# Kernel tuning notes

Measured on AMD Instinct MI355X. Metric: run time of the kernel, lower is better.

The kernel has to match this reference:

```python
import jax, jax.numpy as jnp
import numpy as np

N_NODES = 100000
N_EDGES = 1600000
N_GRAPH = 100
IN_DIM = 64
LATENT = 128
STEPS = 2
MLP_LAYERS = 2
OUT_GLOBALS = 1
EPS = 1e-5  # haiku LayerNorm default


def setup_inputs() -> dict:
    key = jax.random.key(0)
    ks = jax.random.split(key, 8)
    nodes = jax.random.normal(ks[0], (N_NODES, IN_DIM), jnp.float32)
    senders = jax.random.randint(ks[1], (N_EDGES,), 0, N_NODES, jnp.int32)
    receivers = jax.random.randint(ks[2], (N_EDGES,), 0, N_NODES, jnp.int32)
    # 100 graphs of 1000 nodes each: jnp.repeat(arange(n_graph), n_node)
    graph_ids = (jnp.arange(N_NODES) // (N_NODES // N_GRAPH)).astype(jnp.int32)
    embed_w = jax.random.normal(ks[3], (IN_DIM, LATENT), jnp.float32) / np.sqrt(IN_DIM).astype(np.float32)
    embed_b = jnp.zeros((LATENT,), jnp.float32)
    mlp_w = jax.random.normal(ks[4], (STEPS, MLP_LAYERS, LATENT, LATENT), jnp.float32) / np.sqrt(LATENT).astype(np.float32)
    mlp_b = jnp.zeros((STEPS, MLP_LAYERS, LATENT), jnp.float32)
    ln_scale = jnp.ones((STEPS, LATENT), jnp.float32)
    ln_offset = jnp.zeros((STEPS, LATENT), jnp.float32)
    dec_w = jax.random.normal(ks[5], (LATENT, OUT_GLOBALS), jnp.float32) / np.sqrt(LATENT).astype(np.float32)
    dec_b = jnp.zeros((OUT_GLOBALS,), jnp.float32)
    return dict(nodes=nodes, senders=senders, receivers=receivers, graph_ids=graph_ids,
                embed_w=embed_w, embed_b=embed_b, mlp_w=mlp_w, mlp_b=mlp_b,
                ln_scale=ln_scale, ln_offset=ln_offset, dec_w=dec_w, dec_b=dec_b)


def _layernorm(x, scale, offset):
    mu = jnp.mean(x, axis=-1, keepdims=True)
    var = jnp.var(x, axis=-1, keepdims=True)
    return (x - mu) * jax.lax.rsqrt(var + EPS) * scale + offset


def reference(nodes, senders, receivers, graph_ids, embed_w, embed_b,
              mlp_w, mlp_b, ln_scale, ln_offset, dec_w, dec_b):
    n = nodes.shape[0]
    # jraph.GraphConvolution(add_self_edges=True, symmetric_normalization=True)
    self_loop = jnp.arange(n, dtype=senders.dtype)
    conv_s = jnp.concatenate([senders, self_loop])
    conv_r = jnp.concatenate([receivers, self_loop])
    ones_e = jnp.ones(conv_s.shape[0], jnp.float32)
    inv_sqrt_sdeg = jax.lax.rsqrt(jnp.maximum(jax.ops.segment_sum(ones_e, conv_s, n), 1.0))
    inv_sqrt_rdeg = jax.lax.rsqrt(jnp.maximum(jax.ops.segment_sum(ones_e, conv_r, n), 1.0))

    # embedder: hk.Linear on nodes
    h = nodes @ embed_w + embed_b

    for s in range(STEPS):
        # update_node_fn: MLP (dropout_rate=0 -> identity dropout)
        x = h
        for l in range(MLP_LAYERS):
            x = jax.nn.relu(x @ mlp_w[s, l] + mlp_b[s, l])
        # symmetric-normalized segment_sum aggregation with self-edges
        x = x * inv_sqrt_sdeg[:, None]
        x = jax.ops.segment_sum(x[conv_s], conv_r, num_segments=n)  # [n, LATENT]
        x = x * inv_sqrt_rdeg[:, None]
        h = x + h  # skip connection (add_graphs_tuples)
        h = _layernorm(h, ln_scale[s], ln_offset[s])

    # segment_mean pooling over graphs
    counts = jnp.maximum(jax.ops.segment_sum(jnp.ones(n, jnp.float32), graph_ids, N_GRAPH), 1.0)
    pooled = jax.ops.segment_sum(h, graph_ids, num_segments=N_GRAPH) / counts[:, None]
    # decoder: hk.Linear on pooled globals
    return pooled @ dec_w + dec_b  # [N_GRAPH, OUT_GLOBALS]
```

## Files before the change

### kernel.cpp

```cpp
#include <hip/hip_runtime.h>
#include <hip/hip_bf16.h>


#define N_NODES 100000
#define N_EDGES 1600000
#define N_GRAPH 100
#define NPG     1000
#define LATENT  128

#define NPART   8
#define PSIZE   (N_NODES / NPART)
#define NSLICE  32
#define ESLICE  (N_EDGES / NSLICE)

#define SCAN_CHUNK 2048
#define SCAN_NB    ((N_NODES + SCAN_CHUNK - 1) / SCAN_CHUNK)

#define PCHUNK  20
#define PCNODES (NPG / PCHUNK)

typedef __attribute__((ext_vector_type(8))) short short8;
typedef __attribute__((ext_vector_type(4))) float f32x4;

__device__ __forceinline__ unsigned short f2bf(float f) {
    union { float f; unsigned int u; } v; v.f = f;
    unsigned int r = v.u + 0x7fff + ((v.u >> 16) & 1);
    return (unsigned short)(r >> 16);
}
__device__ __forceinline__ float bf2f(unsigned short u) {
    union { unsigned int u; float f; } v; v.u = ((unsigned int)u) << 16;
    return v.f;
}

__global__ __launch_bounds__(1024) void k_hist2(const int* __restrict__ senders,
                                                const int* __restrict__ receivers,
                                                int* __restrict__ ps,
                                                int* __restrict__ pr) {
    __shared__ int cs[PSIZE];
    __shared__ int cr[PSIZE];
    int rg = blockIdx.x & (NPART - 1), sl = blockIdx.x >> 3;
    int lo = rg * PSIZE;
    for (int i = threadIdx.x; i < PSIZE; i += 1024) { cs[i] = 0; cr[i] = 0; }
    __syncthreads();
    int e0 = sl * ESLICE;
    for (int e = e0 + threadIdx.x; e < e0 + ESLICE; e += 1024) {
        int s = senders[e] - lo;
        if ((unsigned)s < PSIZE) atomicAdd(&cs[s], 1);
        int r = receivers[e] - lo;
        if ((unsigned)r < PSIZE) atomicAdd(&cr[r], 1);
    }
    __syncthreads();
    int base = (rg * NSLICE + sl) * PSIZE;
    for (int i = threadIdx.x; i < PSIZE; i += 1024) {
        ps[base + i] = cs[i];
        pr[base + i] = cr[i];
    }
}

__global__ __launch_bounds__(256) void k_scan_slices(const int* __restrict__ ps,
                                                     int* __restrict__ pr,
                                                     int* __restrict__ deg_r,
                                                     float* __restrict__ inv_s,
                                                     float* __restrict__ inv_r) {
    int n = blockIdx.x * 256 + threadIdx.x;
    if (n >= N_NODES) return;
    int rg = n / PSIZE, i = n - rg * PSIZE;
    size_t base = (size_t)rg * NSLICE * PSIZE + i;
    int run = 0, ss = 0;
#pragma unroll 4
    for (int sl = 0; sl < NSLICE; sl++) {
        size_t idx = base + (size_t)sl * PSIZE;
        int v = pr[idx];
        pr[idx] = run;
        run += v;
        ss += ps[idx];
    }
    deg_r[n] = run;
    inv_r[n] = rsqrtf((float)(run + 1));
    inv_s[n] = rsqrtf((float)(ss + 1));
}

__global__ __launch_bounds__(256) void k_scan_block(const int* __restrict__ deg,
                                                    int* __restrict__ blocksums, int n) {
    int b = blockIdx.x, t = threadIdx.x;
    int base = b * SCAN_CHUNK + t * 8;
    int s = 0;
#pragma unroll
    for (int j = 0; j < 8; j++) { int i = base + j; if (i < n) s += deg[i]; }
    __shared__ int wsum[4];
#pragma unroll
    for (int off = 32; off > 0; off >>= 1) s += __shfl_down(s, off, 64);
    if ((t & 63) == 0) wsum[t >> 6] = s;
    __syncthreads();
    if (t == 0) blocksums[b] = wsum[0] + wsum[1] + wsum[2] + wsum[3];
}

__global__ __launch_bounds__(64) void k_scan_top(int* __restrict__ blocksums, int nb) {
    int t = threadIdx.x;
    int v = (t < nb) ? blocksums[t] : 0;
    int inc = v;
#pragma unroll
    for (int off = 1; off < 64; off <<= 1) {
        int u = __shfl_up(inc, off, 64);
        if (t >= off) inc += u;
    }
    if (t < nb) blocksums[t] = inc - v;
}

__global__ __launch_bounds__(256) void k_scan_apply(const int* __restrict__ deg,
                                                    const int* __restrict__ blockoffs,
                                                    int* __restrict__ row_start, int n) {
    int b = blockIdx.x, t = threadIdx.x;
    int base = b * SCAN_CHUNK + t * 8;
    int v[8]; int tsum = 0;
#pragma unroll
    for (int j = 0; j < 8; j++) { int i = base + j; v[j] = (i < n) ? deg[i] : 0; tsum += v[j]; }
    __shared__ int wtot[4];
    int inc = tsum;
#pragma unroll
    for (int off = 1; off < 64; off <<= 1) {
        int u = __shfl_up(inc, off, 64);
        if ((t & 63) >= off) inc += u;
    }
    if ((t & 63) == 63) wtot[t >> 6] = inc;
    __syncthreads();
    int wbase = 0;
    for (int w = 0; w < (t >> 6); w++) wbase += wtot[w];
    int running = blockoffs[b] + wbase + (inc - tsum);
#pragma unroll
    for (int j = 0; j < 8; j++) {
        int i = base + j;
        if (i < n) {
            row_start[i] = running;
            running += v[j];
            if (i == n - 1) row_start[n] = running;
        }
    }
}

__global__ void k_mkbase(int* __restrict__ pr, const int* __restrict__ row_start) {
    int idx = blockIdx.x * 256 + threadIdx.x;
    if (idx >= NPART * NSLICE * PSIZE) return;
    int rg = idx / (NSLICE * PSIZE);
    int i = idx % PSIZE;
    pr[idx] += row_start[rg * PSIZE + i];
}

__global__ __launch_bounds__(1024) void k_fill2(const int* __restrict__ senders,
                                                const int* __restrict__ receivers,
                                                const int* __restrict__ baseoff,
                                                int* __restrict__ edge_src) {
    __shared__ int bs[PSIZE];
    int rg = blockIdx.x & (NPART - 1), sl = blockIdx.x >> 3;
    int lo = rg * PSIZE;
    const int* base = baseoff + (size_t)(rg * NSLICE + sl) * PSIZE;
    for (int i = threadIdx.x; i < PSIZE; i += 1024) bs[i] = base[i];
    __syncthreads();
    int e0 = sl * ESLICE;
    for (int e = e0 + threadIdx.x; e < e0 + ESLICE; e += 1024) {
        int r = receivers[e] - lo;
        if ((unsigned)r < PSIZE) {
            int pos = atomicAdd(&bs[r], 1);
            edge_src[pos] = senders[e];
        }
    }
}

__global__ void k_wprep(const float* __restrict__ embed_w, const float* __restrict__ mlp_w,
                        unsigned short* __restrict__ hi, unsigned short* __restrict__ lo) {
    int t = blockIdx.x * 256 + threadIdx.x;
    if (t >= 8192 + 4 * 16384) return;
    const float* src; int local;
    if (t < 8192) { src = embed_w; local = t; }
    else { int m = t - 8192; src = mlp_w + (size_t)(m >> 14) * 16384; local = m & 16383; }
    int j = local & 7, lane = (local >> 3) & 63, tn = (local >> 9) & 7, kc = local >> 12;
    int k = kc * 32 + ((lane >> 4) << 3) + j;
    int n = tn * 16 + (lane & 15);
    float wv = src[k * 128 + n];
    unsigned short h = f2bf(wv);
    float rem = wv - bf2f(h);
    hi[t] = h; lo[t] = f2bf(rem);
}

__global__ __launch_bounds__(256) void k_embed(
    const float* __restrict__ A, const unsigned short* __restrict__ wfhi,
    const unsigned short* __restrict__ wflo, const float* __restrict__ eb,
    unsigned short* __restrict__ h16, int M)
{
    __shared__ __align__(16) unsigned short t0[4][32][136];
    int t = threadIdx.x, w = t >> 6, L = t & 63;
    int m0 = blockIdx.x * 128 + w * 32;
    int lr = L & 15, lk = (L >> 4) * 8, lq = (L >> 4) * 4;

    float ebv[8];
#pragma unroll
    for (int tn = 0; tn < 8; tn++) ebv[tn] = eb[tn * 16 + lr];

    f32x4 acc[2][8];
#pragma unroll
    for (int bd = 0; bd < 2; bd++)
#pragma unroll
        for (int tn = 0; tn < 8; tn++) acc[bd][tn] = (f32x4){0.f, 0.f, 0.f, 0.f};

#pragma unroll
    for (int kc = 0; kc < 2; kc++) {
        short8 a[2];
#pragma unroll
        for (int bd = 0; bd < 2; bd++) {
            int grow = m0 + bd * 16 + lr; if (grow >= M) grow = M - 1;
            const float* rp = A + (size_t)grow * 64 + kc * 32 + lk;
            float4 v0 = *(const float4*)rp;
            float4 v1 = *(const float4*)(rp + 4);
            short8 pk;
            pk[0] = (short)f2bf(v0.x); pk[1] = (short)f2bf(v0.y);
            pk[2] = (short)f2bf(v0.z); pk[3] = (short)f2bf(v0.w);
            pk[4] = (short)f2bf(v1.x); pk[5] = (short)f2bf(v1.y);
            pk[6] = (short)f2bf(v1.z); pk[7] = (short)f2bf(v1.w);
            a[bd] = pk;
        }
#pragma unroll
        for (int tn = 0; tn < 8; tn++) {
            size_t fo = (size_t)(((kc * 8 + tn) * 64 + L)) * 8;
            short8 bh = *(const short8*)(wfhi + fo);
            short8 bl = *(const short8*)(wflo + fo);
#pragma unroll
            for (int bd = 0; bd < 2; bd++) {
                acc[bd][tn] = __builtin_amdgcn_mfma_f32_16x16x32_bf16(a[bd], bh, acc[bd][tn], 0, 0, 0);
                acc[bd][tn] = __builtin_amdgcn_mfma_f32_16x16x32_bf16(a[bd], bl, acc[bd][tn], 0, 0, 0);
            }
        }
    }
#pragma unroll
    for (int bd = 0; bd < 2; bd++)
#pragma unroll
        for (int tn = 0; tn < 8; tn++)
#pragma unroll
            for (int r = 0; r < 4; r++)
                t0[w][bd * 16 + lq + r][tn * 16 + lr] = f2bf(acc[bd][tn][r] + ebv[tn]);
#pragma unroll
    for (int q = 0; q < 8; q++) {
        int s = q * 64 + L;
        int row = s >> 4, c0 = (s & 15) * 8;
        int grow = m0 + row;
        if (grow < M)
            *(short8*)(h16 + (size_t)grow * 128 + c0) = *(const short8*)&t0[w][row][c0];
    }
}

__global__ __launch_bounds__(256) void k_mlp(
    const unsigned short* __restrict__ A16, const unsigned short* __restrict__ w0hi,
    const unsigned short* __restrict__ w0lo, const unsigned short* __restrict__ w1hi,
    const unsigned short* __restrict__ w1lo, const float* __restrict__ b0,
    const float* __restrict__ b1, const float* __restrict__ inv_s,
    unsigned short* __restrict__ x16, int M)
{
    __shared__ __align__(16) unsigned short t1[4][32][136];
    int t = threadIdx.x, w = t >> 6, L = t & 63;
    int m0 = blockIdx.x * 128 + w * 32;
    int lr = L & 15, lk = (L >> 4) * 8, lq = (L >> 4) * 4;

    float b0v[8], b1v[8];
#pragma unroll
    for (int tn = 0; tn < 8; tn++) { b0v[tn] = b0[tn * 16 + lr]; b1v[tn] = b1[tn * 16 + lr]; }

    f32x4 acc[2][8];
#pragma unroll
    for (int bd = 0; bd < 2; bd++)
#pragma unroll
        for (int tn = 0; tn < 8; tn++) acc[bd][tn] = (f32x4){0.f, 0.f, 0.f, 0.f};

#pragma unroll
    for (int kc = 0; kc < 4; kc++) {
        short8 a[2];
#pragma unroll
        for (int bd = 0; bd < 2; bd++) {
            int grow = m0 + bd * 16 + lr; if (grow >= M) grow = M - 1;
            a[bd] = *(const short8*)(A16 + (size_t)grow * 128 + kc * 32 + lk);
        }
#pragma unroll
        for (int tn = 0; tn < 8; tn++) {
            size_t fo = (size_t)(((kc * 8 + tn) * 64 + L)) * 8;
            short8 bh = *(const short8*)(w0hi + fo);
            short8 bl = *(const short8*)(w0lo + fo);
#pragma unroll
            for (int bd = 0; bd < 2; bd++) {
                acc[bd][tn] = __builtin_amdgcn_mfma_f32_16x16x32_bf16(a[bd], bh, acc[bd][tn], 0, 0, 0);
                acc[bd][tn] = __builtin_amdgcn_mfma_f32_16x16x32_bf16(a[bd], bl, acc[bd][tn], 0, 0, 0);
            }
        }
    }
#pragma unroll
    for (int bd = 0; bd < 2; bd++)
#pragma unroll
        for (int tn = 0; tn < 8; tn++)
#pragma unroll
            for (int r = 0; r < 4; r++) {
                float v = acc[bd][tn][r] + b0v[tn];
                v = fmaxf(v, 0.f);
                t1[w][bd * 16 + lq + r][tn * 16 + lr] = f2bf(v);
            }

    f32x4 acc2[2][8];
#pragma unroll
    for (int bd = 0; bd < 2; bd++)
#pragma unroll
        for (int tn = 0; tn < 8; tn++) acc2[bd][tn] = (f32x4){0.f, 0.f, 0.f, 0.f};

#pragma unroll
    for (int kc = 0; kc < 4; kc++) {
        short8 a[2];
#pragma unroll
        for (int bd = 0; bd < 2; bd++)
            a[bd] = *(const short8*)&t1[w][bd * 16 + lr][kc * 32 + lk];
#pragma unroll
        for (int tn = 0; tn < 8; tn++) {
            size_t fo = (size_t)(((kc * 8 + tn) * 64 + L)) * 8;
            short8 bh = *(const short8*)(w1hi + fo);
            short8 bl = *(const short8*)(w1lo + fo);
#pragma unroll
            for (int bd = 0; bd < 2; bd++) {
                acc2[bd][tn] = __builtin_amdgcn_mfma_f32_16x16x32_bf16(a[bd], bh, acc2[bd][tn], 0, 0, 0);
                acc2[bd][tn] = __builtin_amdgcn_mfma_f32_16x16x32_bf16(a[bd], bl, acc2[bd][tn], 0, 0, 0);
            }
        }
    }

    float invs[2][4];
#pragma unroll
    for (int bd = 0; bd < 2; bd++)
#pragma unroll
        for (int r = 0; r < 4; r++) {
            int grow = m0 + bd * 16 + lq + r; if (grow >= M) grow = M - 1;
            invs[bd][r] = inv_s[grow];
        }
#pragma unroll
    for (int bd = 0; bd < 2; bd++)
#pragma unroll
        for (int tn = 0; tn < 8; tn++)
#pragma unroll
            for (int r = 0; r < 4; r++) {
                float v = acc2[bd][tn][r] + b1v[tn];
                v = fmaxf(v, 0.f) * invs[bd][r];
                t1[w][bd * 16 + lq + r][tn * 16 + lr] = f2bf(v);
            }
#pragma unroll
    for (int q = 0; q < 8; q++) {
        int s = q * 64 + L;
        int row = s >> 4;
        int c0 = (s & 15) * 8;
        int grow = m0 + row;
        if (grow < M)
            *(short8*)(x16 + (size_t)grow * 128 + c0) = *(const short8*)&t1[w][row][c0];
    }
}

__global__ __launch_bounds__(256) void k_agg_ln(
    const unsigned short* __restrict__ x16, const int* __restrict__ row_start,
    const int* __restrict__ edge_src, const float* __restrict__ inv_r,
    const float* __restrict__ ln_scale, const float* __restrict__ ln_offset,
    unsigned short* __restrict__ h16)
{
    int node = __builtin_amdgcn_readfirstlane(blockIdx.x * 4 + (threadIdx.x >> 6));
    int L = threadIdx.x & 63;
    const unsigned int* x32 = (const unsigned int*)x16;
    const unsigned int* h32 = (const unsigned int*)h16;

    unsigned int su = x32[(size_t)node * 64 + L];
    float a0 = bf2f((unsigned short)(su & 0xffff));
    float a1 = bf2f((unsigned short)(su >> 16));

    int beg = row_start[node], end = row_start[node + 1];
    int j = beg;
    for (; j + 8 <= end; j += 8) {
        unsigned int u[8];
#pragma unroll
        for (int q = 0; q < 8; q++) u[q] = x32[(size_t)edge_src[j + q] * 64 + L];
#pragma unroll
        for (int q = 0; q < 8; q++) {
            a0 += bf2f((unsigned short)(u[q] & 0xffff));
            a1 += bf2f((unsigned short)(u[q] >> 16));
        }
    }
    for (; j < end; j++) {
        unsigned int u0 = x32[(size_t)edge_src[j] * 64 + L];
        a0 += bf2f((unsigned short)(u0 & 0xffff));
        a1 += bf2f((unsigned short)(u0 >> 16));
    }

    float ir = inv_r[node];
    unsigned int hu = h32[(size_t)node * 64 + L];
    float y0 = a0 * ir + bf2f((unsigned short)(hu & 0xffff));
    float y1 = a1 * ir + bf2f((unsigned short)(hu >> 16));

    float s1 = y0 + y1, s2 = y0 * y0 + y1 * y1;
#pragma unroll
    for (int off = 32; off > 0; off >>= 1) {
        s1 += __shfl_xor(s1, off, 64);
        s2 += __shfl_xor(s2, off, 64);
    }
    float mu = s1 * (1.f / 128.f);
    float var = fmaxf(s2 * (1.f / 128.f) - mu * mu, 0.f);
    float rstd = rsqrtf(var + 1e-5f);
    float2 sc = *(const float2*)&ln_scale[L * 2];
    float2 of = *(const float2*)&ln_offset[L * 2];
    float ox = (y0 - mu) * rstd * sc.x + of.x;
    float oy = (y1 - mu) * rstd * sc.y + of.y;
    ((unsigned int*)h16)[(size_t)node * 64 + L] =
        (unsigned int)f2bf(ox) | ((unsigned int)f2bf(oy) << 16);
}

__global__ __launch_bounds__(256) void k_pool1(const unsigned short* __restrict__ h16,
                                               float* __restrict__ partial) {
    int b = blockIdx.x;
    int g = b / PCHUNK, c = b % PCHUNK;
    int t = threadIdx.x, col = t & 127, half = t >> 7;
    const unsigned short* hg = h16 + ((size_t)g * NPG + (size_t)c * PCNODES) * 128;
    float acc = 0.f;
    for (int i = half; i < PCNODES; i += 2) acc += bf2f(hg[(size_t)i * 128 + col]);
    __shared__ float red[256];
    red[t] = acc;
    __syncthreads();
    if (half == 0) partial[(size_t)b * 128 + col] = red[col] + red[col + 128];
}

__global__ __launch_bounds__(128) void k_pool2(const float* __restrict__ partial,
                                               const float* __restrict__ dec_w,
                                               const float* __restrict__ dec_b,
                                               float* __restrict__ out) {
    int g = blockIdx.x, col = threadIdx.x;
    const float* pg = partial + (size_t)g * PCHUNK * 128;
    float s = 0.f;
#pragma unroll
    for (int c = 0; c < PCHUNK; c++) s += pg[c * 128 + col];
    s = s * (1.f / (float)NPG) * dec_w[col];
    __shared__ float ws[2];
#pragma unroll
    for (int off = 32; off > 0; off >>= 1) s += __shfl_down(s, off, 64);
    if ((col & 63) == 0) ws[col >> 6] = s;
    __syncthreads();
    if (col == 0) out[g] = ws[0] + ws[1] + dec_b[0];
}

extern "C" void kernel_launch(void* const* d_in, const int* in_sizes, int n_in,
                              void* d_out, int out_size, void* d_ws, size_t ws_size,
                              hipStream_t stream) {
    (void)in_sizes; (void)n_in; (void)out_size; (void)ws_size;
    const float* nodes     = (const float*)d_in[0];
    const int*   senders   = (const int*)d_in[1];
    const int*   receivers = (const int*)d_in[2];
    const float* embed_w   = (const float*)d_in[4];
    const float* embed_b   = (const float*)d_in[5];
    const float* mlp_w     = (const float*)d_in[6];
    const float* mlp_b     = (const float*)d_in[7];
    const float* ln_scale  = (const float*)d_in[8];
    const float* ln_offset = (const float*)d_in[9];
    const float* dec_w     = (const float*)d_in[10];
    const float* dec_b     = (const float*)d_in[11];
    float* out = (float*)d_out;

    const int N = N_NODES;
    const int WF_TOTAL = 8192 + 4 * 16384;
    const int PART_TOTAL = NPART * NSLICE * PSIZE;

    char* p = (char*)d_ws;
    auto alloc = [&](size_t bytes) -> void* {
        void* r = (void*)p;
        p += (bytes + 255) & ~(size_t)255;
        return r;
    };
    unsigned short* h16      = (unsigned short*)alloc((size_t)N * 128 * 2);
    unsigned short* x16      = (unsigned short*)alloc((size_t)N * 128 * 2);
    int*            edge_src = (int*)alloc((size_t)N_EDGES * 4);
    int*            ps       = (int*)alloc((size_t)PART_TOTAL * 4);
    int*            pr       = (int*)alloc((size_t)PART_TOTAL * 4);
    int*            deg_r    = (int*)alloc((size_t)N * 4);
    float*          inv_s    = (float*)alloc((size_t)N * 4);
    float*          inv_r    = (float*)alloc((size_t)N * 4);
    int*            row_start= (int*)alloc((size_t)(N + 1) * 4);
    int*            blocksums= (int*)alloc((size_t)SCAN_NB * 4);
    unsigned short* wfhi     = (unsigned short*)alloc((size_t)WF_TOTAL * 2);
    unsigned short* wflo     = (unsigned short*)alloc((size_t)WF_TOTAL * 2);
    float*          poolpart = (float*)alloc((size_t)N_GRAPH * PCHUNK * 128 * 4);

    k_wprep<<<(WF_TOTAL + 255) / 256, 256, 0, stream>>>(embed_w, mlp_w, wfhi, wflo);

    k_hist2<<<NPART * NSLICE, 1024, 0, stream>>>(senders, receivers, ps, pr);
    k_scan_slices<<<(N + 255) / 256, 256, 0, stream>>>(ps, pr, deg_r, inv_s, inv_r);
    k_scan_block<<<SCAN_NB, 256, 0, stream>>>(deg_r, blocksums, N);
    k_scan_top<<<1, 64, 0, stream>>>(blocksums, SCAN_NB);
    k_scan_apply<<<SCAN_NB, 256, 0, stream>>>(deg_r, blocksums, row_start, N);
    k_mkbase<<<(PART_TOTAL + 255) / 256, 256, 0, stream>>>(pr, row_start);
    k_fill2<<<NPART * NSLICE, 1024, 0, stream>>>(senders, receivers, pr, edge_src);

    int mblocks = (N + 127) / 128;
    k_embed<<<mblocks, 256, 0, stream>>>(nodes, wfhi, wflo, embed_b, h16, N);

    for (int s = 0; s < 2; s++) {
        const unsigned short* w0hi = wfhi + 8192 + (size_t)(s * 2 + 0) * 16384;
        const unsigned short* w0lo = wflo + 8192 + (size_t)(s * 2 + 0) * 16384;
        const unsigned short* w1hi = wfhi + 8192 + (size_t)(s * 2 + 1) * 16384;
        const unsigned short* w1lo = wflo + 8192 + (size_t)(s * 2 + 1) * 16384;
        const float* b0 = mlp_b + (size_t)(s * 2 + 0) * 128;
        const float* b1 = mlp_b + (size_t)(s * 2 + 1) * 128;
        k_mlp<<<mblocks, 256, 0, stream>>>(h16, w0hi, w0lo, w1hi, w1lo, b0, b1, inv_s, x16, N);
        k_agg_ln<<<N / 4, 256, 0, stream>>>(x16, row_start, edge_src, inv_r,
                                            ln_scale + (size_t)s * 128,
                                            ln_offset + (size_t)s * 128, h16);
    }

    k_pool1<<<N_GRAPH * PCHUNK, 256, 0, stream>>>(h16, poolpart);
    k_pool2<<<N_GRAPH, 128, 0, stream>>>(poolpart, dec_w, dec_b, out);
}
```

Baseline: 436.4 us.

## Fuse embedder into first MLP step, shrink partition counters to u16, drop mkbase

The embedding GEMM and the step-0 two-layer MLP now run in one kernel. The embedded tile stays in LDS as the A operand, so the separate reload of h16 is avoided. Per-slice histogram counters are stored as 16-bit values, and the base-offset addition moves into k_fill2, which removes the k_mkbase launch and halves the partition buffer traffic. The bf16 unpacking in aggregation is simplified to bit shifts and masks. One risk is that 16-bit running sums could overflow if a receiver's in-degree ever reached 65536.

```diff
diff --git a/kernel.cpp b/kernel.cpp
--- a/kernel.cpp
+++ b/kernel.cpp
@@ -34,8 +34,8 @@
 
 __global__ __launch_bounds__(1024) void k_hist2(const int* __restrict__ senders,
                                                 const int* __restrict__ receivers,
-                                                int* __restrict__ ps,
-                                                int* __restrict__ pr) {
+                                                unsigned short* __restrict__ ps16,
+                                                unsigned short* __restrict__ pr16) {
     __shared__ int cs[PSIZE];
     __shared__ int cr[PSIZE];
     int rg = blockIdx.x & (NPART - 1), sl = blockIdx.x >> 3;
@@ -50,15 +50,15 @@
         if ((unsigned)r < PSIZE) atomicAdd(&cr[r], 1);
     }
     __syncthreads();
-    int base = (rg * NSLICE + sl) * PSIZE;
+    size_t base = (size_t)(rg * NSLICE + sl) * PSIZE;
     for (int i = threadIdx.x; i < PSIZE; i += 1024) {
-        ps[base + i] = cs[i];
-        pr[base + i] = cr[i];
-    }
-}
-
-__global__ __launch_bounds__(256) void k_scan_slices(const int* __restrict__ ps,
-                                                     int* __restrict__ pr,
+        ps16[base + i] = (unsigned short)cs[i];
+        pr16[base + i] = (unsigned short)cr[i];
+    }
+}
+
+__global__ __launch_bounds__(256) void k_scan_slices(const unsigned short* __restrict__ ps16,
+                                                     unsigned short* __restrict__ pr16,
                                                      int* __restrict__ deg_r,
                                                      float* __restrict__ inv_s,
                                                      float* __restrict__ inv_r) {
@@ -70,10 +70,10 @@
 #pragma unroll 4
     for (int sl = 0; sl < NSLICE; sl++) {
         size_t idx = base + (size_t)sl * PSIZE;
-        int v = pr[idx];
-        pr[idx] = run;
+        int v = pr16[idx];
+        pr16[idx] = (unsigned short)run;
         run += v;
-        ss += ps[idx];
+        ss += ps16[idx];
     }
     deg_r[n] = run;
     inv_r[n] = rsqrtf((float)(run + 1));
@@ -138,23 +138,17 @@
     }
 }
 
-__global__ void k_mkbase(int* __restrict__ pr, const int* __restrict__ row_start) {
-    int idx = blockIdx.x * 256 + threadIdx.x;
-    if (idx >= NPART * NSLICE * PSIZE) return;
-    int rg = idx / (NSLICE * PSIZE);
-    int i = idx % PSIZE;
-    pr[idx] += row_start[rg * PSIZE + i];
-}
-
 __global__ __launch_bounds__(1024) void k_fill2(const int* __restrict__ senders,
                                                 const int* __restrict__ receivers,
-                                                const int* __restrict__ baseoff,
+                                                const unsigned short* __restrict__ pr16,
+                                                const int* __restrict__ row_start,
                                                 int* __restrict__ edge_src) {
     __shared__ int bs[PSIZE];
     int rg = blockIdx.x & (NPART - 1), sl = blockIdx.x >> 3;
     int lo = rg * PSIZE;
-    const int* base = baseoff + (size_t)(rg * NSLICE + sl) * PSIZE;
-    for (int i = threadIdx.x; i < PSIZE; i += 1024) bs[i] = base[i];
+    const unsigned short* base = pr16 + (size_t)(rg * NSLICE + sl) * PSIZE;
+    for (int i = threadIdx.x; i < PSIZE; i += 1024)
+        bs[i] = row_start[lo + i] + (int)base[i];
     __syncthreads();
     int e0 = sl * ESLICE;
     for (int e = e0 + threadIdx.x; e < e0 + ESLICE; e += 1024) {
@@ -182,26 +176,34 @@
     hi[t] = h; lo[t] = f2bf(rem);
 }
 
-__global__ __launch_bounds__(256) void k_embed(
-    const float* __restrict__ A, const unsigned short* __restrict__ wfhi,
-    const unsigned short* __restrict__ wflo, const float* __restrict__ eb,
-    unsigned short* __restrict__ h16, int M)
+__global__ __launch_bounds__(256) void k_embed_mlp(
+    const float* __restrict__ A,
+    const unsigned short* __restrict__ wehi, const unsigned short* __restrict__ welo,
+    const float* __restrict__ eb,
+    const unsigned short* __restrict__ w0hi, const unsigned short* __restrict__ w0lo,
+    const unsigned short* __restrict__ w1hi, const unsigned short* __restrict__ w1lo,
+    const float* __restrict__ b0, const float* __restrict__ b1,
+    const float* __restrict__ inv_s,
+    unsigned short* __restrict__ h16, unsigned short* __restrict__ x16, int M)
 {
     __shared__ __align__(16) unsigned short t0[4][32][136];
     int t = threadIdx.x, w = t >> 6, L = t & 63;
     int m0 = blockIdx.x * 128 + w * 32;
     int lr = L & 15, lk = (L >> 4) * 8, lq = (L >> 4) * 4;
 
-    float ebv[8];
-#pragma unroll
-    for (int tn = 0; tn < 8; tn++) ebv[tn] = eb[tn * 16 + lr];
+    float ebv[8], b0v[8], b1v[8];
+#pragma unroll
+    for (int tn = 0; tn < 8; tn++) {
+        ebv[tn] = eb[tn * 16 + lr];
+        b0v[tn] = b0[tn * 16 + lr];
+        b1v[tn] = b1[tn * 16 + lr];
+    }
 
     f32x4 acc[2][8];
 #pragma unroll
     for (int bd = 0; bd < 2; bd++)
 #pragma unroll
         for (int tn = 0; tn < 8; tn++) acc[bd][tn] = (f32x4){0.f, 0.f, 0.f, 0.f};
-
 #pragma unroll
     for (int kc = 0; kc < 2; kc++) {
         short8 a[2];
@@ -221,8 +223,8 @@
 #pragma unroll
         for (int tn = 0; tn < 8; tn++) {
             size_t fo = (size_t)(((kc * 8 + tn) * 64 + L)) * 8;
-            short8 bh = *(const short8*)(wfhi + fo);
-            short8 bl = *(const short8*)(wflo + fo);
+            short8 bh = *(const short8*)(wehi + fo);
+            short8 bl = *(const short8*)(welo + fo);
 #pragma unroll
             for (int bd = 0; bd < 2; bd++) {
                 acc[bd][tn] = __builtin_amdgcn_mfma_f32_16x16x32_bf16(a[bd], bh, acc[bd][tn], 0, 0, 0);
@@ -244,6 +246,83 @@
         int grow = m0 + row;
         if (grow < M)
             *(short8*)(h16 + (size_t)grow * 128 + c0) = *(const short8*)&t0[w][row][c0];
+    }
+
+#pragma unroll
+    for (int bd = 0; bd < 2; bd++)
+#pragma unroll
+        for (int tn = 0; tn < 8; tn++) acc[bd][tn] = (f32x4){0.f, 0.f, 0.f, 0.f};
+#pragma unroll
+    for (int kc = 0; kc < 4; kc++) {
+        short8 a[2];
+#pragma unroll
+        for (int bd = 0; bd < 2; bd++)
+            a[bd] = *(const short8*)&t0[w][bd * 16 + lr][kc * 32 + lk];
+#pragma unroll
+        for (int tn = 0; tn < 8; tn++) {
+            size_t fo = (size_t)(((kc * 8 + tn) * 64 + L)) * 8;
+            short8 bh = *(const short8*)(w0hi + fo);
+            short8 bl = *(const short8*)(w0lo + fo);
+#pragma unroll
+            for (int bd = 0; bd < 2; bd++) {
+                acc[bd][tn] = __builtin_amdgcn_mfma_f32_16x16x32_bf16(a[bd], bh, acc[bd][tn], 0, 0, 0);
+                acc[bd][tn] = __builtin_amdgcn_mfma_f32_16x16x32_bf16(a[bd], bl, acc[bd][tn], 0, 0, 0);
+            }
+        }
+    }
+#pragma unroll
+    for (int bd = 0; bd < 2; bd++)
+#pragma unroll
+        for (int tn = 0; tn < 8; tn++)
+#pragma unroll
+            for (int r = 0; r < 4; r++)
+                t0[w][bd * 16 + lq + r][tn * 16 + lr] = f2bf(fmaxf(acc[bd][tn][r] + b0v[tn], 0.f));
+
+#pragma unroll
+    for (int bd = 0; bd < 2; bd++)
+#pragma unroll
+        for (int tn = 0; tn < 8; tn++) acc[bd][tn] = (f32x4){0.f, 0.f, 0.f, 0.f};
+#pragma unroll
+    for (int kc = 0; kc < 4; kc++) {
+        short8 a[2];
+#pragma unroll
+        for (int bd = 0; bd < 2; bd++)
+            a[bd] = *(const short8*)&t0[w][bd * 16 + lr][kc * 32 + lk];
+#pragma unroll
+        for (int tn = 0; tn < 8; tn++) {
+            size_t fo = (size_t)(((kc * 8 + tn) * 64 + L)) * 8;
+            short8 bh = *(const short8*)(w1hi + fo);
+            short8 bl = *(const short8*)(w1lo + fo);
+#pragma unroll
+            for (int bd = 0; bd < 2; bd++) {
+                acc[bd][tn] = __builtin_amdgcn_mfma_f32_16x16x32_bf16(a[bd], bh, acc[bd][tn], 0, 0, 0);
+                acc[bd][tn] = __builtin_amdgcn_mfma_f32_16x16x32_bf16(a[bd], bl, acc[bd][tn], 0, 0, 0);
+            }
+        }
+    }
+    float invs[2][4];
+#pragma unroll
+    for (int bd = 0; bd < 2; bd++)
+#pragma unroll
+        for (int r = 0; r < 4; r++) {
+            int grow = m0 + bd * 16 + lq + r; if (grow >= M) grow = M - 1;
+            invs[bd][r] = inv_s[grow];
+        }
+#pragma unroll
+    for (int bd = 0; bd < 2; bd++)
+#pragma unroll
+        for (int tn = 0; tn < 8; tn++)
+#pragma unroll
+            for (int r = 0; r < 4; r++)
+                t0[w][bd * 16 + lq + r][tn * 16 + lr] =
+                    f2bf(fmaxf(acc[bd][tn][r] + b1v[tn], 0.f) * invs[bd][r]);
+#pragma unroll
+    for (int q = 0; q < 8; q++) {
+        int s = q * 64 + L;
+        int row = s >> 4, c0 = (s & 15) * 8;
+        int grow = m0 + row;
+        if (grow < M)
+            *(short8*)(x16 + (size_t)grow * 128 + c0) = *(const short8*)&t0[w][row][c0];
     }
 }
 
@@ -294,18 +373,14 @@
 #pragma unroll
         for (int tn = 0; tn < 8; tn++)
 #pragma unroll
-            for (int r = 0; r < 4; r++) {
-                float v = acc[bd][tn][r] + b0v[tn];
-                v = fmaxf(v, 0.f);
-                t1[w][bd * 16 + lq + r][tn * 16 + lr] = f2bf(v);
-            }
+            for (int r = 0; r < 4; r++)
+                t1[w][bd * 16 + lq + r][tn * 16 + lr] = f2bf(fmaxf(acc[bd][tn][r] + b0v[tn], 0.f));
 
     f32x4 acc2[2][8];
 #pragma unroll
     for (int bd = 0; bd < 2; bd++)
 #pragma unroll
         for (int tn = 0; tn < 8; tn++) acc2[bd][tn] = (f32x4){0.f, 0.f, 0.f, 0.f};
-
 #pragma unroll
     for (int kc = 0; kc < 4; kc++) {
         short8 a[2];
@@ -324,7 +399,6 @@
             }
         }
     }
-
     float invs[2][4];
 #pragma unroll
     for (int bd = 0; bd < 2; bd++)
@@ -338,16 +412,13 @@
 #pragma unroll
         for (int tn = 0; tn < 8; tn++)
 #pragma unroll
-            for (int r = 0; r < 4; r++) {
-                float v = acc2[bd][tn][r] + b1v[tn];
-                v = fmaxf(v, 0.f) * invs[bd][r];
-                t1[w][bd * 16 + lq + r][tn * 16 + lr] = f2bf(v);
-            }
+            for (int r = 0; r < 4; r++)
+                t1[w][bd * 16 + lq + r][tn * 16 + lr] =
+                    f2bf(fmaxf(acc2[bd][tn][r] + b1v[tn], 0.f) * invs[bd][r]);
 #pragma unroll
     for (int q = 0; q < 8; q++) {
         int s = q * 64 + L;
-        int row = s >> 4;
-        int c0 = (s & 15) * 8;
+        int row = s >> 4, c0 = (s & 15) * 8;
         int grow = m0 + row;
         if (grow < M)
             *(short8*)(x16 + (size_t)grow * 128 + c0) = *(const short8*)&t1[w][row][c0];
@@ -366,8 +437,9 @@
     const unsigned int* h32 = (const unsigned int*)h16;
 
     unsigned int su = x32[(size_t)node * 64 + L];
-    float a0 = bf2f((unsigned short)(su & 0xffff));
-    float a1 = bf2f((unsigned short)(su >> 16));
+    float2 acc;
+    acc.x = __uint_as_float(su << 16);
+    acc.y = __uint_as_float(su & 0xffff0000u);
 
     int beg = row_start[node], end = row_start[node + 1];
     int j = beg;
@@ -377,20 +449,20 @@
         for (int q = 0; q < 8; q++) u[q] = x32[(size_t)edge_src[j + q] * 64 + L];
 #pragma unroll
         for (int q = 0; q < 8; q++) {
-            a0 += bf2f((unsigned short)(u[q] & 0xffff));
-            a1 += bf2f((unsigned short)(u[q] >> 16));
+            acc.x += __uint_as_float(u[q] << 16);
+            acc.y += __uint_as_float(u[q] & 0xffff0000u);
         }
     }
     for (; j < end; j++) {
         unsigned int u0 = x32[(size_t)edge_src[j] * 64 + L];
-        a0 += bf2f((unsigned short)(u0 & 0xffff));
-        a1 += bf2f((unsigned short)(u0 >> 16));
+        acc.x += __uint_as_float(u0 << 16);
+        acc.y += __uint_as_float(u0 & 0xffff0000u);
     }
 
     float ir = inv_r[node];
     unsigned int hu = h32[(size_t)node * 64 + L];
-    float y0 = a0 * ir + bf2f((unsigned short)(hu & 0xffff));
-    float y1 = a1 * ir + bf2f((unsigned short)(hu >> 16));
+    float y0 = acc.x * ir + __uint_as_float(hu << 16);
+    float y1 = acc.y * ir + __uint_as_float(hu & 0xffff0000u);
 
     float s1 = y0 + y1, s2 = y0 * y0 + y1 * y1;
 #pragma unroll
@@ -471,8 +543,8 @@
     unsigned short* h16      = (unsigned short*)alloc((size_t)N * 128 * 2);
     unsigned short* x16      = (unsigned short*)alloc((size_t)N * 128 * 2);
     int*            edge_src = (int*)alloc((size_t)N_EDGES * 4);
-    int*            ps       = (int*)alloc((size_t)PART_TOTAL * 4);
-    int*            pr       = (int*)alloc((size_t)PART_TOTAL * 4);
+    unsigned short* ps16     = (unsigned short*)alloc((size_t)PART_TOTAL * 2);
+    unsigned short* pr16     = (unsigned short*)alloc((size_t)PART_TOTAL * 2);
     int*            deg_r    = (int*)alloc((size_t)N * 4);
     float*          inv_s    = (float*)alloc((size_t)N * 4);
     float*          inv_r    = (float*)alloc((size_t)N * 4);
@@ -484,29 +556,29 @@
 
     k_wprep<<<(WF_TOTAL + 255) / 256, 256, 0, stream>>>(embed_w, mlp_w, wfhi, wflo);
 
-    k_hist2<<<NPART * NSLICE, 1024, 0, stream>>>(senders, receivers, ps, pr);
-    k_scan_slices<<<(N + 255) / 256, 256, 0, stream>>>(ps, pr, deg_r, inv_s, inv_r);
+    k_hist2<<<NPART * NSLICE, 1024, 0, stream>>>(senders, receivers, ps16, pr16);
+    k_scan_slices<<<(N + 255) / 256, 256, 0, stream>>>(ps16, pr16, deg_r, inv_s, inv_r);
     k_scan_block<<<SCAN_NB, 256, 0, stream>>>(deg_r, blocksums, N);
     k_scan_top<<<1, 64, 0, stream>>>(blocksums, SCAN_NB);
     k_scan_apply<<<SCAN_NB, 256, 0, stream>>>(deg_r, blocksums, row_start, N);
-    k_mkbase<<<(PART_TOTAL + 255) / 256, 256, 0, stream>>>(pr, row_start);
-    k_fill2<<<NPART * NSLICE, 1024, 0, stream>>>(senders, receivers, pr, edge_src);
+    k_fill2<<<NPART * NSLICE, 1024, 0, stream>>>(senders, receivers, pr16, row_start, edge_src);
 
     int mblocks = (N + 127) / 128;
-    k_embed<<<mblocks, 256, 0, stream>>>(nodes, wfhi, wflo, embed_b, h16, N);
-
-    for (int s = 0; s < 2; s++) {
-        const unsigned short* w0hi = wfhi + 8192 + (size_t)(s * 2 + 0) * 16384;
-        const unsigned short* w0lo = wflo + 8192 + (size_t)(s * 2 + 0) * 16384;
-        const unsigned short* w1hi = wfhi + 8192 + (size_t)(s * 2 + 1) * 16384;
-        const unsigned short* w1lo = wflo + 8192 + (size_t)(s * 2 + 1) * 16384;
-        const float* b0 = mlp_b + (size_t)(s * 2 + 0) * 128;
-        const float* b1 = mlp_b + (size_t)(s * 2 + 1) * 128;
-        k_mlp<<<mblocks, 256, 0, stream>>>(h16, w0hi, w0lo, w1hi, w1lo, b0, b1, inv_s, x16, N);
-        k_agg_ln<<<N / 4, 256, 0, stream>>>(x16, row_start, edge_src, inv_r,
-                                            ln_scale + (size_t)s * 128,
-                                            ln_offset + (size_t)s * 128, h16);
-    }
+    const unsigned short* wehi = wfhi, *welo = wflo;
+    const unsigned short* w0hi[2] = { wfhi + 8192,             wfhi + 8192 + 2 * 16384 };
+    const unsigned short* w0lo[2] = { wflo + 8192,             wflo + 8192 + 2 * 16384 };
+    const unsigned short* w1hi[2] = { wfhi + 8192 + 16384,     wfhi + 8192 + 3 * 16384 };
+    const unsigned short* w1lo[2] = { wflo + 8192 + 16384,     wflo + 8192 + 3 * 16384 };
+
+    k_embed_mlp<<<mblocks, 256, 0, stream>>>(nodes, wehi, welo, embed_b,
+                                             w0hi[0], w0lo[0], w1hi[0], w1lo[0],
+                                             mlp_b, mlp_b + 128, inv_s, h16, x16, N);
+    k_agg_ln<<<N / 4, 256, 0, stream>>>(x16, row_start, edge_src, inv_r,
+                                        ln_scale, ln_offset, h16);
+    k_mlp<<<mblocks, 256, 0, stream>>>(h16, w0hi[1], w0lo[1], w1hi[1], w1lo[1],
+                                       mlp_b + 256, mlp_b + 384, inv_s, x16, N);
+    k_agg_ln<<<N / 4, 256, 0, stream>>>(x16, row_start, edge_src, inv_r,
+                                        ln_scale + 128, ln_offset + 128, h16);
 
     k_pool1<<<N_GRAPH * PCHUNK, 256, 0, stream>>>(h16, poolpart);
     k_pool2<<<N_GRAPH, 128, 0, stream>>>(poolpart, dec_w, dec_b, out);
```

Result: faster. 423.3 us (-3.0%).
